# Kernel optimization log

Measured on AMD Instinct MI355X. Metric: run time of the kernel, lower is better.

## Reference

```python
import jax, jax.numpy as jnp
import numpy as np

N, M, K = 4, 50, 240000
POS_THRESH = 0.7
NEG_THRESH = 0.3
RPN_BATCH = 512
NUM_FG = RPN_BATCH // 2
NUM_BG = RPN_BATCH - NUM_FG
NEG_INF = -1e9


def setup_inputs() -> dict:
    key = jax.random.key(0)
    k1, k2, k3, k4, k5, k6 = jax.random.split(key, 6)
    # anchors: valid boxes (x1,y1,x2,y2) inside a ~960x600 image
    a_xy = jax.random.uniform(k1, (K, 2)) * jnp.array([900.0, 550.0])
    a_wh = jax.random.uniform(k2, (K, 2)) * 120.0 + 16.0
    anchors = jnp.concatenate([a_xy, a_xy + a_wh], axis=-1)
    g_xy = jax.random.uniform(k3, (N, M, 2)) * jnp.array([900.0, 550.0])
    g_wh = jax.random.uniform(k4, (N, M, 2)) * 120.0 + 16.0
    gt_boxes = jnp.concatenate([g_xy, g_xy + g_wh], axis=-1)
    rpn_cls_score = jax.random.normal(k5, (N, K))
    gt_labels = jax.random.randint(k6, (N, M), 1, 3, dtype=jnp.int32)
    return {"anchors": anchors, "rpn_cls_score": rpn_cls_score,
            "gt_boxes": gt_boxes, "gt_labels": gt_labels}


def _iou(anchors, gt_boxes):
    # anchors (K,4), gt_boxes (N,M,4) -> (N,K,M)
    a = anchors[None, :, None, :]   # (1,K,1,4)
    g = gt_boxes[:, None, :, :]     # (N,1,M,4)
    lt = jnp.maximum(a[..., :2], g[..., :2])
    rb = jnp.minimum(a[..., 2:], g[..., 2:])
    wh = jnp.clip(rb - lt, 0.0)
    inter = wh[..., 0] * wh[..., 1]
    area_a = (a[..., 2] - a[..., 0]) * (a[..., 3] - a[..., 1])
    area_g = (g[..., 2] - g[..., 0]) * (g[..., 3] - g[..., 1])
    return inter / (area_a + area_g - inter + 1e-8)


def _encode(anchors, matched):
    # anchors (K,4), matched (N,K,4) -> (N,K,4) standard (dx,dy,dw,dh)
    aw = anchors[:, 2] - anchors[:, 0]
    ah = anchors[:, 3] - anchors[:, 1]
    acx = anchors[:, 0] + 0.5 * aw
    acy = anchors[:, 1] + 0.5 * ah
    gw = matched[..., 2] - matched[..., 0]
    gh = matched[..., 3] - matched[..., 1]
    gcx = matched[..., 0] + 0.5 * gw
    gcy = matched[..., 1] + 0.5 * gh
    return jnp.stack([(gcx - acx) / aw, (gcy - acy) / ah,
                      jnp.log(gw / aw), jnp.log(gh / ah)], axis=-1)


def _subsample_one(score, pos, neg):
    # deterministic balanced sampler: top NUM_FG positives and top NUM_BG
    # negatives ranked by objectness criterion (hard mining)
    pos_key = jnp.where(pos, score, NEG_INF)
    neg_key = jnp.where(neg, score, NEG_INF)
    pv, pi = jax.lax.top_k(pos_key, NUM_FG)
    nv, ni = jax.lax.top_k(neg_key, NUM_BG)
    mask = jnp.zeros(score.shape[0], dtype=score.dtype)
    mask = mask.at[pi].max((pv > NEG_INF / 2).astype(score.dtype))
    mask = mask.at[ni].max((nv > NEG_INF / 2).astype(score.dtype))
    return mask


def reference(anchors, rpn_cls_score, gt_boxes, gt_labels):
    ious = _iou(anchors, gt_boxes)                 # (N,K,M)
    max_o = jnp.max(ious, axis=-1)                 # (N,K)
    argm = jnp.argmax(ious, axis=-1)               # (N,K)
    pos = max_o >= POS_THRESH
    neg = max_o < NEG_THRESH
    matched = jnp.take_along_axis(
        gt_boxes, jnp.broadcast_to(argm[:, :, None], (N, K, 4)), axis=1)
    matched_labels = jnp.take_along_axis(gt_labels, argm, axis=1)
    cls_targets = jnp.where(pos, matched_labels, 0)
    reg_targets = _encode(anchors, matched) * pos[..., None].astype(anchors.dtype)
    cls_weights = (pos | neg).astype(anchors.dtype)
    reg_weights = pos.astype(anchors.dtype)
    mask = jax.vmap(_subsample_one)(rpn_cls_score, pos, neg)  # (N,K)
    cls_weights = cls_weights * mask
    reg_weights = reg_weights * mask
    return cls_targets, reg_targets, cls_weights, reg_weights
```

## Files before the change

kernel.cpp:

```cpp
#include <hip/hip_runtime.h>

#define KA 240000
#define NI 4
#define MG 50
#define NSEL 256u
#define CAPL 4096
#define BPI 235
#define GRID (BPI * NI)

typedef unsigned int u32;

#define METAO 16384
#define LISTO (METAO + 32)
#define ONE_F 0x3F800000u

static __device__ __forceinline__ u32 sortkey32(float f) {
    u32 b = __float_as_uint(f);
    return (b & 0x80000000u) ? ~b : (b | 0x80000000u);
}
static __device__ __forceinline__ void patch1(u32* p) {
    __hip_atomic_store(p, ONE_F, __ATOMIC_RELAXED, __HIP_MEMORY_SCOPE_AGENT);
}

extern "C" __global__ void __launch_bounds__(256, 4)
AnchorTargetLayer_48052094107725_kernel(
    const float4* __restrict__ anchors, const float* __restrict__ scores,
    const float4* __restrict__ gtb, const int* __restrict__ glab,
    float* __restrict__ out, u32* __restrict__ flags, u32* __restrict__ ws) {
#pragma clang fp contract(off)
    __shared__ float4 gA[MG];
    __shared__ int glb[MG];
    __shared__ u32 lh[2048];
    const int bx = blockIdx.x;
    const int tid = threadIdx.x;
    const int n = bx / BPI;
    const int kb = bx - n * BPI;

    if (tid < 18) {
        const int i = bx * 18 + tid;
        if (i < LISTO) atomicExch(&ws[i], 0u);
    }
    for (int i = tid; i < 2048; i += 256) lh[i] = 0;
    if (tid < MG) {
        gA[tid] = gtb[n * MG + tid];
        glb[tid] = glab[n * MG + tid];
    }
    __syncthreads();

    const int k0 = (kb * 256 + tid) * 4;
    if (k0 < KA) {
        float ax0[4], ay0[4], ax2[4], ay2[4];
        #pragma unroll
        for (int j = 0; j < 4; ++j) {
            const float4 A = anchors[k0 + j];
            ax0[j] = A.x; ay0[j] = A.y; ax2[j] = A.z; ay2[j] = A.w;
        }
        float aaw[4], aah[4], aar[4], bst[4];
        int bix[4];
        #pragma unroll
        for (int j = 0; j < 4; ++j) {
            aaw[j] = ax2[j] - ax0[j];
            aah[j] = ay2[j] - ay0[j];
            aar[j] = aaw[j] * aah[j];
            bst[j] = -1.0f;
            bix[j] = 0;
        }
        for (int m = 0; m < MG; m += 2) {
            const float4 Ga = gA[m];
            const float4 Gb = gA[m + 1];
            const float gaA = (Ga.z - Ga.x) * (Ga.w - Ga.y);
            const float gaB = (Gb.z - Gb.x) * (Gb.w - Gb.y);
            #pragma unroll
            for (int j = 0; j < 4; ++j) {
                const float wa = fmaxf(fminf(ax2[j], Ga.z) - fmaxf(ax0[j], Ga.x), 0.0f);
                const float ha = fmaxf(fminf(ay2[j], Ga.w) - fmaxf(ay0[j], Ga.y), 0.0f);
                const float ia = wa * ha;
                const float qa = ia / (((aar[j] + gaA) - ia) + 1e-8f);
                const float wb = fmaxf(fminf(ax2[j], Gb.z) - fmaxf(ax0[j], Gb.x), 0.0f);
                const float hb = fmaxf(fminf(ay2[j], Gb.w) - fmaxf(ay0[j], Gb.y), 0.0f);
                const float ib = wb * hb;
                const float qb = ib / (((aar[j] + gaB) - ib) + 1e-8f);
                if (qa > bst[j]) { bst[j] = qa; bix[j] = m; }
                if (qb > bst[j]) { bst[j] = qb; bix[j] = m + 1; }
            }
        }

        const int nk = n * KA + k0;
        const float4 s4 = ((const float4*)scores)[nk >> 2];
        const float scv[4] = {s4.x, s4.y, s4.z, s4.w};

        float clsv[4];
        float4 regv[4];
        u32 flagpack = 0;
        #pragma unroll
        for (int j = 0; j < 4; ++j) {
            const bool pos = bst[j] >= 0.7f;
            const bool neg = bst[j] < 0.3f;
            clsv[j] = pos ? (float)glb[bix[j]] : 0.0f;
            float4 rv = make_float4(0.0f, 0.0f, 0.0f, 0.0f);
            if (pos) {
                const float4 Gm = gA[bix[j]];
                const float gw = Gm.z - Gm.x, gh = Gm.w - Gm.y;
                const float gcx = Gm.x + 0.5f * gw, gcy = Gm.y + 0.5f * gh;
                const float acx = ax0[j] + 0.5f * aaw[j], acy = ay0[j] + 0.5f * aah[j];
                rv.x = (gcx - acx) / aaw[j];
                rv.y = (gcy - acy) / aah[j];
                rv.z = logf(gw / aaw[j]);
                rv.w = logf(gh / aah[j]);
            }
            regv[j] = rv;
            const u32 fl = pos ? 1u : (neg ? 2u : 0u);
            flagpack |= fl << (8 * j);
            if (fl) atomicAdd(&lh[sortkey32(scv[j]) >> 21], fl == 2u ? 0x10000u : 1u);
        }
        const size_t NK = (size_t)NI * KA;
        const size_t NK4 = NK / 4;
        const int t4 = nk >> 2;
        ((float4*)out)[t4] = make_float4(clsv[0], clsv[1], clsv[2], clsv[3]);
        float4* regp = ((float4*)(out + NK)) + nk;
        regp[0] = regv[0]; regp[1] = regv[1]; regp[2] = regv[2]; regp[3] = regv[3];
        const float4 z4 = make_float4(0.0f, 0.0f, 0.0f, 0.0f);
        ((float4*)out)[5 * NK4 + t4] = z4;
        ((float4*)out)[6 * NK4 + t4] = z4;
        flags[t4] = flagpack;
    }
    __syncthreads();
    const int gp = 2 * n;
    for (int i = tid; i < 2048; i += 256) {
        const u32 c = lh[i];
        if (c & 0xFFFFu) atomicAdd(&ws[gp * 2048 + i], c & 0xFFFFu);
        if (c >> 16)     atomicAdd(&ws[(gp + 1) * 2048 + i], c >> 16);
    }
}

__global__ void __launch_bounds__(256) kP(const float* __restrict__ scores,
                                          const u32* __restrict__ flagsW,
                                          u32* __restrict__ ws,
                                          float* __restrict__ out) {
    __shared__ u32 cs[256];
    __shared__ u32 s_us[2], s_R[2], s_done[2];
    const int bx = blockIdx.x, tid = threadIdx.x;
    const int n = bx / BPI, kb = bx - n * BPI;
    u32* hist = ws;
    u32* meta = ws + METAO;
    u32* list = ws + LISTO;

    for (int gi = 0; gi < 2; ++gi) {
        const int g = 2 * n + gi;
        u32 loc[8];
        u32 s = 0;
        const int base = g * 2048 + tid * 8;
        #pragma unroll
        for (int j = 0; j < 8; ++j) { loc[j] = hist[base + j]; s += loc[j]; }
        cs[tid] = s;
        __syncthreads();
        for (int d = 1; d < 256; d <<= 1) {
            const u32 add = (tid + d < 256) ? cs[tid + d] : 0u;
            __syncthreads();
            cs[tid] += add;
            __syncthreads();
        }
        if (tid == 0) s_done[gi] = (cs[0] < NSEL) ? 1u : 0u;
        u32 run = (tid < 255) ? cs[tid + 1] : 0u;
        #pragma unroll
        for (int j = 7; j >= 0; --j) {
            const u32 Sj = run + loc[j];
            if (Sj >= NSEL && run < NSEL) {
                s_us[gi] = (u32)(tid * 8 + j);
                s_R[gi] = NSEL - run;
            }
            run = Sj;
        }
        __syncthreads();
    }
    if (kb == 0 && tid == 0) {
        meta[2 * n] = s_us[0];     meta[8 + 2 * n] = s_R[0];     meta[16 + 2 * n] = s_done[0];
        meta[2 * n + 1] = s_us[1]; meta[8 + 2 * n + 1] = s_R[1]; meta[16 + 2 * n + 1] = s_done[1];
    }

    const int k0 = (kb * 256 + tid) * 4;
    if (k0 >= KA) return;
    const int nk = n * KA + k0;
    const u32 fw = flagsW[nk >> 2];
    if (!fw) return;
    const float4 s4 = ((const float4*)scores)[nk >> 2];
    const float scv[4] = {s4.x, s4.y, s4.z, s4.w};
    const size_t NK = (size_t)NI * KA;
    u32* o32 = (u32*)out;
    #pragma unroll
    for (int j = 0; j < 4; ++j) {
        const u32 f = (fw >> (8 * j)) & 255u;
        if (!f) continue;
        const int gi = (f == 2u) ? 1 : 0;
        bool in = false;
        if (s_done[gi]) {
            in = true;
        } else {
            const u32 key = sortkey32(scv[j]);
            const u32 p11 = key >> 21;
            if (p11 > s_us[gi]) {
                in = true;
            } else if (p11 == s_us[gi]) {
                const int g = 2 * n + gi;
                const u32 p = atomicAdd(&meta[24 + g], 1u);
                if (p < CAPL) {
                    list[(g * CAPL + p) * 2] = key;
                    list[(g * CAPL + p) * 2 + 1] = (u32)(k0 + j);
                }
            }
        }
        if (in) {
            patch1(&o32[5 * NK + nk + j]);
            if (f == 1u) patch1(&o32[6 * NK + nk + j]);
        }
    }
}

__global__ void __launch_bounds__(256) kR2(const u32* __restrict__ ws,
                                           float* __restrict__ out) {
    __shared__ u32 h2[1024];
    __shared__ u32 cs[256];
    __shared__ u32 s_usb, s_R2, s_tc;
    __shared__ u32 tk[256], ti[256];
    const u32* meta = ws + METAO;
    const u32* list = ws + LISTO;
    const int g = blockIdx.x, tid = threadIdx.x;
    if (meta[16 + g]) return;
    u32 c = meta[24 + g];
    if (c > CAPL) c = CAPL;
    const u32 R1 = meta[8 + g];
    for (u32 i = tid; i < 1024; i += 256) h2[i] = 0;
    if (tid == 0) s_tc = 0;
    __syncthreads();
    for (u32 j = tid; j < c; j += 256)
        atomicAdd(&h2[(list[(g * CAPL + j) * 2] >> 11) & 1023u], 1u);
    __syncthreads();
    u32 loc[4];
    u32 s = 0;
    #pragma unroll
    for (int j = 0; j < 4; ++j) { loc[j] = h2[tid * 4 + j]; s += loc[j]; }
    cs[tid] = s;
    __syncthreads();
    for (int d = 1; d < 256; d <<= 1) {
        const u32 add = (tid + d < 256) ? cs[tid + d] : 0u;
        __syncthreads();
        cs[tid] += add;
        __syncthreads();
    }
    u32 run = (tid < 255) ? cs[tid + 1] : 0u;
    #pragma unroll
    for (int j = 3; j >= 0; --j) {
        const u32 Sj = run + loc[j];
        if (Sj >= R1 && run < R1) { s_usb = (u32)(tid * 4 + j); s_R2 = R1 - run; }
        run = Sj;
    }
    __syncthreads();
    const u32 usb = s_usb, R2 = s_R2;
    const int nn = g >> 1;
    const bool posg = ((g & 1) == 0);
    const size_t NK = (size_t)NI * KA;
    u32* o32 = (u32*)out;
    for (u32 j = tid; j < c; j += 256) {
        const u32 key = list[(g * CAPL + j) * 2];
        const u32 idx = list[(g * CAPL + j) * 2 + 1];
        const u32 sb = (key >> 11) & 1023u;
        if (sb > usb) {
            const size_t o = (size_t)nn * KA + idx;
            patch1(&o32[5 * NK + o]);
            if (posg) patch1(&o32[6 * NK + o]);
        } else if (sb == usb) {
            const u32 p = atomicAdd(&s_tc, 1u);
            if (p < 256) { tk[p] = key; ti[p] = idx; }
        }
    }
    __syncthreads();
    u32 tc = s_tc;
    if (tc > 256) tc = 256;
    for (u32 i = tid; i < tc; i += 256) {
        const u32 ki = tk[i], ii = ti[i];
        u32 rank = 0;
        for (u32 j = 0; j < tc; ++j) {
            const u32 kj = tk[j];
            if (kj > ki || (kj == ki && ti[j] < ii)) rank++;
        }
        if (rank < R2) {
            const size_t o = (size_t)nn * KA + ii;
            patch1(&o32[5 * NK + o]);
            if (posg) patch1(&o32[6 * NK + o]);
        }
    }
}

extern "C" void kernel_launch(void* const* d_in, const int* in_sizes, int n_in,
                              void* d_out, int out_size, void* d_ws, size_t ws_size,
                              hipStream_t stream) {
    (void)in_sizes; (void)n_in; (void)out_size; (void)ws_size;
    const float4* anchors = (const float4*)d_in[0];
    const float*  scores  = (const float*)d_in[1];
    const float4* gtb     = (const float4*)d_in[2];
    const int*    glab    = (const int*)d_in[3];
    float* out = (float*)d_out;

    u32* ws = (u32*)d_ws;
    u32* flags = ws + LISTO + 8 * CAPL * 2;

    AnchorTargetLayer_48052094107725_kernel<<<GRID, 256, 0, stream>>>(
        anchors, scores, gtb, glab, out, flags, ws);
    kP<<<GRID, 256, 0, stream>>>(scores, flags, ws, out);
    kR2<<<8, 256, 0, stream>>>(ws, out);
}
```

Baseline: 137.1 us.

## Fuse histogram scan and refinement into last-block tails, doubling anchors per thread

Each thread now handles eight anchors instead of four, which halves the grid and adds a per-block precomputed GT area table. The histogram prefix scan moves from every kP block into the last-arriving block of the first kernel, chosen with an atomic ticket counter. The kR2 refinement pass is folded into the last-arriving block of kP. This removes one launch and the redundant per-block scans, at the cost of serialising the tail work of all eight groups onto a single block and doubling register pressure per thread.

```diff
diff --git a/kernel.cpp b/kernel.cpp
--- a/kernel.cpp
+++ b/kernel.cpp
@@ -5,18 +5,27 @@
 #define MG 50
 #define NSEL 256u
 #define CAPL 4096
-#define BPI 235
-#define GRID (BPI * NI)
+#define APT 8
+#define BPI 118
+#define GRID1 (BPI * NI)
 
 typedef unsigned int u32;
 
 #define METAO 16384
-#define LISTO (METAO + 32)
+#define TICKO (METAO + 32)
+#define LISTO (TICKO + 2)
+#define FLAGO (LISTO + 8 * CAPL * 2)
 #define ONE_F 0x3F800000u
 
 static __device__ __forceinline__ u32 sortkey32(float f) {
     u32 b = __float_as_uint(f);
     return (b & 0x80000000u) ? ~b : (b | 0x80000000u);
+}
+static __device__ __forceinline__ u32 aload(const u32* p) {
+    return __hip_atomic_load(p, __ATOMIC_ACQUIRE, __HIP_MEMORY_SCOPE_AGENT);
+}
+static __device__ __forceinline__ void astore(u32* p, u32 v) {
+    __hip_atomic_store(p, v, __ATOMIC_RELEASE, __HIP_MEMORY_SCOPE_AGENT);
 }
 static __device__ __forceinline__ void patch1(u32* p) {
     __hip_atomic_store(p, ONE_F, __ATOMIC_RELAXED, __HIP_MEMORY_SCOPE_AGENT);
@@ -26,74 +35,74 @@
 AnchorTargetLayer_48052094107725_kernel(
     const float4* __restrict__ anchors, const float* __restrict__ scores,
     const float4* __restrict__ gtb, const int* __restrict__ glab,
-    float* __restrict__ out, u32* __restrict__ flags, u32* __restrict__ ws) {
+    float* __restrict__ out, u32* __restrict__ ws) {
 #pragma clang fp contract(off)
     __shared__ float4 gA[MG];
+    __shared__ float gare[MG];
     __shared__ int glb[MG];
     __shared__ u32 lh[2048];
+    __shared__ u32 cs[256];
+    __shared__ u32 s_tick;
     const int bx = blockIdx.x;
     const int tid = threadIdx.x;
     const int n = bx / BPI;
     const int kb = bx - n * BPI;
 
-    if (tid < 18) {
-        const int i = bx * 18 + tid;
+    if (tid < 35) {
+        const int i = bx * 35 + tid;
         if (i < LISTO) atomicExch(&ws[i], 0u);
     }
     for (int i = tid; i < 2048; i += 256) lh[i] = 0;
     if (tid < MG) {
-        gA[tid] = gtb[n * MG + tid];
+        const float4 G = gtb[n * MG + tid];
+        gA[tid] = G;
+        gare[tid] = (G.z - G.x) * (G.w - G.y);
         glb[tid] = glab[n * MG + tid];
     }
     __syncthreads();
 
-    const int k0 = (kb * 256 + tid) * 4;
+    const int k0 = (kb * 256 + tid) * APT;
     if (k0 < KA) {
-        float ax0[4], ay0[4], ax2[4], ay2[4];
-        #pragma unroll
-        for (int j = 0; j < 4; ++j) {
+        float ax0[APT], ay0[APT], ax2[APT], ay2[APT];
+        #pragma unroll
+        for (int j = 0; j < APT; ++j) {
             const float4 A = anchors[k0 + j];
             ax0[j] = A.x; ay0[j] = A.y; ax2[j] = A.z; ay2[j] = A.w;
         }
-        float aaw[4], aah[4], aar[4], bst[4];
-        int bix[4];
-        #pragma unroll
-        for (int j = 0; j < 4; ++j) {
+        float aaw[APT], aah[APT], aar[APT], bst[APT];
+        int bix[APT];
+        #pragma unroll
+        for (int j = 0; j < APT; ++j) {
             aaw[j] = ax2[j] - ax0[j];
             aah[j] = ay2[j] - ay0[j];
             aar[j] = aaw[j] * aah[j];
             bst[j] = -1.0f;
             bix[j] = 0;
         }
-        for (int m = 0; m < MG; m += 2) {
+        for (int m = 0; m < MG; ++m) {
             const float4 Ga = gA[m];
-            const float4 Gb = gA[m + 1];
-            const float gaA = (Ga.z - Ga.x) * (Ga.w - Ga.y);
-            const float gaB = (Gb.z - Gb.x) * (Gb.w - Gb.y);
+            const float gaA = gare[m];
             #pragma unroll
-            for (int j = 0; j < 4; ++j) {
+            for (int j = 0; j < APT; ++j) {
                 const float wa = fmaxf(fminf(ax2[j], Ga.z) - fmaxf(ax0[j], Ga.x), 0.0f);
                 const float ha = fmaxf(fminf(ay2[j], Ga.w) - fmaxf(ay0[j], Ga.y), 0.0f);
                 const float ia = wa * ha;
                 const float qa = ia / (((aar[j] + gaA) - ia) + 1e-8f);
-                const float wb = fmaxf(fminf(ax2[j], Gb.z) - fmaxf(ax0[j], Gb.x), 0.0f);
-                const float hb = fmaxf(fminf(ay2[j], Gb.w) - fmaxf(ay0[j], Gb.y), 0.0f);
-                const float ib = wb * hb;
-                const float qb = ib / (((aar[j] + gaB) - ib) + 1e-8f);
                 if (qa > bst[j]) { bst[j] = qa; bix[j] = m; }
-                if (qb > bst[j]) { bst[j] = qb; bix[j] = m + 1; }
             }
         }
 
         const int nk = n * KA + k0;
-        const float4 s4 = ((const float4*)scores)[nk >> 2];
-        const float scv[4] = {s4.x, s4.y, s4.z, s4.w};
-
-        float clsv[4];
-        float4 regv[4];
+        const float4 sa = ((const float4*)scores)[nk >> 2];
+        const float4 sb = ((const float4*)scores)[(nk >> 2) + 1];
+        const float scv[APT] = {sa.x, sa.y, sa.z, sa.w, sb.x, sb.y, sb.z, sb.w};
+
+        float clsv[APT];
         u32 flagpack = 0;
-        #pragma unroll
-        for (int j = 0; j < 4; ++j) {
+        const size_t NK = (size_t)NI * KA;
+        float4* regp = ((float4*)(out + NK)) + nk;
+        #pragma unroll
+        for (int j = 0; j < APT; ++j) {
             const bool pos = bst[j] >= 0.7f;
             const bool neg = bst[j] < 0.3f;
             clsv[j] = pos ? (float)glb[bix[j]] : 0.0f;
@@ -108,50 +117,138 @@
                 rv.z = logf(gw / aaw[j]);
                 rv.w = logf(gh / aah[j]);
             }
-            regv[j] = rv;
+            regp[j] = rv;
             const u32 fl = pos ? 1u : (neg ? 2u : 0u);
-            flagpack |= fl << (8 * j);
+            flagpack |= fl << (4 * j);
             if (fl) atomicAdd(&lh[sortkey32(scv[j]) >> 21], fl == 2u ? 0x10000u : 1u);
         }
-        const size_t NK = (size_t)NI * KA;
         const size_t NK4 = NK / 4;
         const int t4 = nk >> 2;
         ((float4*)out)[t4] = make_float4(clsv[0], clsv[1], clsv[2], clsv[3]);
-        float4* regp = ((float4*)(out + NK)) + nk;
-        regp[0] = regv[0]; regp[1] = regv[1]; regp[2] = regv[2]; regp[3] = regv[3];
+        ((float4*)out)[t4 + 1] = make_float4(clsv[4], clsv[5], clsv[6], clsv[7]);
         const float4 z4 = make_float4(0.0f, 0.0f, 0.0f, 0.0f);
         ((float4*)out)[5 * NK4 + t4] = z4;
+        ((float4*)out)[5 * NK4 + t4 + 1] = z4;
         ((float4*)out)[6 * NK4 + t4] = z4;
-        flags[t4] = flagpack;
-    }
-    __syncthreads();
-    const int gp = 2 * n;
-    for (int i = tid; i < 2048; i += 256) {
-        const u32 c = lh[i];
-        if (c & 0xFFFFu) atomicAdd(&ws[gp * 2048 + i], c & 0xFFFFu);
-        if (c >> 16)     atomicAdd(&ws[(gp + 1) * 2048 + i], c >> 16);
-    }
-}
-
-__global__ void __launch_bounds__(256) kP(const float* __restrict__ scores,
-                                          const u32* __restrict__ flagsW,
-                                          u32* __restrict__ ws,
-                                          float* __restrict__ out) {
+        ((float4*)out)[6 * NK4 + t4 + 1] = z4;
+        ws[FLAGO + (nk / APT)] = flagpack;
+    }
+    __syncthreads();
+    {
+        const int gp = 2 * n;
+        for (int i = tid; i < 2048; i += 256) {
+            const u32 c = lh[i];
+            if (c & 0xFFFFu) atomicAdd(&ws[gp * 2048 + i], c & 0xFFFFu);
+            if (c >> 16)     atomicAdd(&ws[(gp + 1) * 2048 + i], c >> 16);
+        }
+    }
+    __threadfence();
+    if (tid == 0) s_tick = atomicAdd(&ws[TICKO], 1u);
+    __syncthreads();
+    if (s_tick == (u32)(GRID1 - 1)) {
+        u32* meta = ws + METAO;
+        for (int g = 0; g < 8; ++g) {
+            u32 loc[8];
+            u32 s = 0;
+            const int base = g * 2048 + tid * 8;
+            #pragma unroll
+            for (int j = 0; j < 8; ++j) { loc[j] = aload(&ws[base + j]); s += loc[j]; }
+            cs[tid] = s;
+            __syncthreads();
+            for (int d = 1; d < 256; d <<= 1) {
+                const u32 add = (tid + d < 256) ? cs[tid + d] : 0u;
+                __syncthreads();
+                cs[tid] += add;
+                __syncthreads();
+            }
+            if (tid == 0) meta[16 + g] = (cs[0] < NSEL) ? 1u : 0u;
+            u32 run = (tid < 255) ? cs[tid + 1] : 0u;
+            #pragma unroll
+            for (int j = 7; j >= 0; --j) {
+                const u32 Sj = run + loc[j];
+                if (Sj >= NSEL && run < NSEL) {
+                    meta[g] = (u32)(tid * 8 + j);
+                    meta[8 + g] = NSEL - run;
+                }
+                run = Sj;
+            }
+            __syncthreads();
+        }
+    }
+}
+
+__global__ void __launch_bounds__(256, 4) kP(const float* __restrict__ scores,
+                                             u32* __restrict__ ws,
+                                             float* __restrict__ out) {
+    __shared__ u32 s_meta[32];
+    __shared__ u32 h2[1024];
     __shared__ u32 cs[256];
-    __shared__ u32 s_us[2], s_R[2], s_done[2];
+    __shared__ u32 tk[256], ti[256];
+    __shared__ u32 s_usb, s_R2, s_tc, s_tick;
+    u32* meta = ws + METAO;
+    u32* list = ws + LISTO;
     const int bx = blockIdx.x, tid = threadIdx.x;
     const int n = bx / BPI, kb = bx - n * BPI;
-    u32* hist = ws;
-    u32* meta = ws + METAO;
-    u32* list = ws + LISTO;
-
-    for (int gi = 0; gi < 2; ++gi) {
-        const int g = 2 * n + gi;
-        u32 loc[8];
+    if (tid < 32) s_meta[tid] = meta[tid];
+    __syncthreads();
+
+    const int k0 = (kb * 256 + tid) * APT;
+    const size_t NK = (size_t)NI * KA;
+    u32* o32 = (u32*)out;
+    if (k0 < KA) {
+        const int nk = n * KA + k0;
+        const u32 fw = ws[FLAGO + (nk / APT)];
+        if (fw) {
+            const float4 sa = ((const float4*)scores)[nk >> 2];
+            const float4 sb = ((const float4*)scores)[(nk >> 2) + 1];
+            const float scv[APT] = {sa.x, sa.y, sa.z, sa.w, sb.x, sb.y, sb.z, sb.w};
+            #pragma unroll
+            for (int j = 0; j < APT; ++j) {
+                const u32 f = (fw >> (4 * j)) & 15u;
+                if (!f) continue;
+                const int g = 2 * n + ((f == 2u) ? 1 : 0);
+                bool in = false;
+                if (s_meta[16 + g]) {
+                    in = true;
+                } else {
+                    const u32 key = sortkey32(scv[j]);
+                    const u32 p11 = key >> 21;
+                    if (p11 > s_meta[g]) {
+                        in = true;
+                    } else if (p11 == s_meta[g]) {
+                        const u32 p = atomicAdd(&meta[24 + g], 1u);
+                        if (p < CAPL) {
+                            astore(&list[(g * CAPL + p) * 2], key);
+                            astore(&list[(g * CAPL + p) * 2 + 1], (u32)(k0 + j));
+                        }
+                    }
+                }
+                if (in) {
+                    patch1(&o32[5 * NK + nk + j]);
+                    if (f == 1u) patch1(&o32[6 * NK + nk + j]);
+                }
+            }
+        }
+    }
+    __threadfence();
+    if (tid == 0) s_tick = atomicAdd(&ws[TICKO + 1], 1u);
+    __syncthreads();
+    if (s_tick != (u32)(GRID1 - 1)) return;
+    for (int g = 0; g < 8; ++g) {
+        if (s_meta[16 + g]) continue;
+        u32 c = aload(&meta[24 + g]);
+        if (c > CAPL) c = CAPL;
+        const u32 R1 = s_meta[8 + g];
+        for (u32 i = tid; i < 1024; i += 256) h2[i] = 0;
+        if (tid == 0) s_tc = 0;
+        __syncthreads();
+        for (u32 j = tid; j < c; j += 256)
+            atomicAdd(&h2[(aload(&list[(g * CAPL + j) * 2]) >> 11) & 1023u], 1u);
+        __syncthreads();
+        u32 loc[4];
         u32 s = 0;
-        const int base = g * 2048 + tid * 8;
-        #pragma unroll
-        for (int j = 0; j < 8; ++j) { loc[j] = hist[base + j]; s += loc[j]; }
+        #pragma unroll
+        for (int j = 0; j < 4; ++j) { loc[j] = h2[tid * 4 + j]; s += loc[j]; }
         cs[tid] = s;
         __syncthreads();
         for (int d = 1; d < 256; d <<= 1) {
@@ -160,134 +257,47 @@
             cs[tid] += add;
             __syncthreads();
         }
-        if (tid == 0) s_done[gi] = (cs[0] < NSEL) ? 1u : 0u;
         u32 run = (tid < 255) ? cs[tid + 1] : 0u;
         #pragma unroll
-        for (int j = 7; j >= 0; --j) {
+        for (int j = 3; j >= 0; --j) {
             const u32 Sj = run + loc[j];
-            if (Sj >= NSEL && run < NSEL) {
-                s_us[gi] = (u32)(tid * 8 + j);
-                s_R[gi] = NSEL - run;
-            }
+            if (Sj >= R1 && run < R1) { s_usb = (u32)(tid * 4 + j); s_R2 = R1 - run; }
             run = Sj;
         }
         __syncthreads();
-    }
-    if (kb == 0 && tid == 0) {
-        meta[2 * n] = s_us[0];     meta[8 + 2 * n] = s_R[0];     meta[16 + 2 * n] = s_done[0];
-        meta[2 * n + 1] = s_us[1]; meta[8 + 2 * n + 1] = s_R[1]; meta[16 + 2 * n + 1] = s_done[1];
-    }
-
-    const int k0 = (kb * 256 + tid) * 4;
-    if (k0 >= KA) return;
-    const int nk = n * KA + k0;
-    const u32 fw = flagsW[nk >> 2];
-    if (!fw) return;
-    const float4 s4 = ((const float4*)scores)[nk >> 2];
-    const float scv[4] = {s4.x, s4.y, s4.z, s4.w};
-    const size_t NK = (size_t)NI * KA;
-    u32* o32 = (u32*)out;
-    #pragma unroll
-    for (int j = 0; j < 4; ++j) {
-        const u32 f = (fw >> (8 * j)) & 255u;
-        if (!f) continue;
-        const int gi = (f == 2u) ? 1 : 0;
-        bool in = false;
-        if (s_done[gi]) {
-            in = true;
-        } else {
-            const u32 key = sortkey32(scv[j]);
-            const u32 p11 = key >> 21;
-            if (p11 > s_us[gi]) {
-                in = true;
-            } else if (p11 == s_us[gi]) {
-                const int g = 2 * n + gi;
-                const u32 p = atomicAdd(&meta[24 + g], 1u);
-                if (p < CAPL) {
-                    list[(g * CAPL + p) * 2] = key;
-                    list[(g * CAPL + p) * 2 + 1] = (u32)(k0 + j);
-                }
-            }
-        }
-        if (in) {
-            patch1(&o32[5 * NK + nk + j]);
-            if (f == 1u) patch1(&o32[6 * NK + nk + j]);
-        }
-    }
-}
-
-__global__ void __launch_bounds__(256) kR2(const u32* __restrict__ ws,
-                                           float* __restrict__ out) {
-    __shared__ u32 h2[1024];
-    __shared__ u32 cs[256];
-    __shared__ u32 s_usb, s_R2, s_tc;
-    __shared__ u32 tk[256], ti[256];
-    const u32* meta = ws + METAO;
-    const u32* list = ws + LISTO;
-    const int g = blockIdx.x, tid = threadIdx.x;
-    if (meta[16 + g]) return;
-    u32 c = meta[24 + g];
-    if (c > CAPL) c = CAPL;
-    const u32 R1 = meta[8 + g];
-    for (u32 i = tid; i < 1024; i += 256) h2[i] = 0;
-    if (tid == 0) s_tc = 0;
-    __syncthreads();
-    for (u32 j = tid; j < c; j += 256)
-        atomicAdd(&h2[(list[(g * CAPL + j) * 2] >> 11) & 1023u], 1u);
-    __syncthreads();
-    u32 loc[4];
-    u32 s = 0;
-    #pragma unroll
-    for (int j = 0; j < 4; ++j) { loc[j] = h2[tid * 4 + j]; s += loc[j]; }
-    cs[tid] = s;
-    __syncthreads();
-    for (int d = 1; d < 256; d <<= 1) {
-        const u32 add = (tid + d < 256) ? cs[tid + d] : 0u;
-        __syncthreads();
-        cs[tid] += add;
-        __syncthreads();
-    }
-    u32 run = (tid < 255) ? cs[tid + 1] : 0u;
-    #pragma unroll
-    for (int j = 3; j >= 0; --j) {
-        const u32 Sj = run + loc[j];
-        if (Sj >= R1 && run < R1) { s_usb = (u32)(tid * 4 + j); s_R2 = R1 - run; }
-        run = Sj;
-    }
-    __syncthreads();
-    const u32 usb = s_usb, R2 = s_R2;
-    const int nn = g >> 1;
-    const bool posg = ((g & 1) == 0);
-    const size_t NK = (size_t)NI * KA;
-    u32* o32 = (u32*)out;
-    for (u32 j = tid; j < c; j += 256) {
-        const u32 key = list[(g * CAPL + j) * 2];
-        const u32 idx = list[(g * CAPL + j) * 2 + 1];
-        const u32 sb = (key >> 11) & 1023u;
-        if (sb > usb) {
-            const size_t o = (size_t)nn * KA + idx;
-            patch1(&o32[5 * NK + o]);
-            if (posg) patch1(&o32[6 * NK + o]);
-        } else if (sb == usb) {
-            const u32 p = atomicAdd(&s_tc, 1u);
-            if (p < 256) { tk[p] = key; ti[p] = idx; }
-        }
-    }
-    __syncthreads();
-    u32 tc = s_tc;
-    if (tc > 256) tc = 256;
-    for (u32 i = tid; i < tc; i += 256) {
-        const u32 ki = tk[i], ii = ti[i];
-        u32 rank = 0;
-        for (u32 j = 0; j < tc; ++j) {
-            const u32 kj = tk[j];
-            if (kj > ki || (kj == ki && ti[j] < ii)) rank++;
-        }
-        if (rank < R2) {
-            const size_t o = (size_t)nn * KA + ii;
-            patch1(&o32[5 * NK + o]);
-            if (posg) patch1(&o32[6 * NK + o]);
-        }
+        const u32 usb = s_usb, R2 = s_R2;
+        const int nn = g >> 1;
+        const bool posg = ((g & 1) == 0);
+        for (u32 j = tid; j < c; j += 256) {
+            const u32 key = aload(&list[(g * CAPL + j) * 2]);
+            const u32 idx = aload(&list[(g * CAPL + j) * 2 + 1]);
+            const u32 sbn = (key >> 11) & 1023u;
+            if (sbn > usb) {
+                const size_t o = (size_t)nn * KA + idx;
+                patch1(&o32[5 * NK + o]);
+                if (posg) patch1(&o32[6 * NK + o]);
+            } else if (sbn == usb) {
+                const u32 p = atomicAdd(&s_tc, 1u);
+                if (p < 256) { tk[p] = key; ti[p] = idx; }
+            }
+        }
+        __syncthreads();
+        u32 tc = s_tc;
+        if (tc > 256) tc = 256;
+        for (u32 i = tid; i < tc; i += 256) {
+            const u32 ki = tk[i], ii = ti[i];
+            u32 rank = 0;
+            for (u32 j = 0; j < tc; ++j) {
+                const u32 kj = tk[j];
+                if (kj > ki || (kj == ki && ti[j] < ii)) rank++;
+            }
+            if (rank < R2) {
+                const size_t o = (size_t)nn * KA + ii;
+                patch1(&o32[5 * NK + o]);
+                if (posg) patch1(&o32[6 * NK + o]);
+            }
+        }
+        __syncthreads();
     }
 }
 
@@ -300,12 +310,9 @@
     const float4* gtb     = (const float4*)d_in[2];
     const int*    glab    = (const int*)d_in[3];
     float* out = (float*)d_out;
-
     u32* ws = (u32*)d_ws;
-    u32* flags = ws + LISTO + 8 * CAPL * 2;
-
-    AnchorTargetLayer_48052094107725_kernel<<<GRID, 256, 0, stream>>>(
-        anchors, scores, gtb, glab, out, flags, ws);
-    kP<<<GRID, 256, 0, stream>>>(scores, flags, ws, out);
-    kR2<<<8, 256, 0, stream>>>(ws, out);
-}
+
+    AnchorTargetLayer_48052094107725_kernel<<<GRID1, 256, 0, stream>>>(
+        anchors, scores, gtb, glab, out, ws);
+    kP<<<GRID1, 256, 0, stream>>>(scores, ws, out);
+}
```

Result: slower. 274.5 us (+100.2%).
